# Performance work log

Measured on AMD Instinct MI355X. Metric: run time of the kernel, lower is better.

The kernel has to match this reference:

```python
import jax, jax.numpy as jnp
import numpy as np

WS = 8      # window_size
NH = 4      # num_heads (fixed in module)

def setup_inputs() -> dict:
    key = jax.random.key(0)
    k1, k2, k3 = jax.random.split(key, 3)
    B, C, H, W = 8, 512, 128, 128
    x = jax.random.normal(k1, (B, C, H, W), dtype=jnp.float32)
    # nn.MultiheadAttention parameters (xavier-ish scale)
    w_in = jax.random.normal(k2, (3 * C, C), dtype=jnp.float32) * (1.0 / np.sqrt(C))
    b_in = jnp.zeros((3 * C,), dtype=jnp.float32)
    w_out = jax.random.normal(k3, (C, C), dtype=jnp.float32) * (1.0 / np.sqrt(C))
    b_out = jnp.zeros((C,), dtype=jnp.float32)
    return {"x": x, "w_in": w_in, "b_in": b_in, "w_out": w_out, "b_out": b_out}

def reference(x, w_in, b_in, w_out, b_out):
    B, C, H, W = x.shape
    Hw, Ww = H // WS, W // WS
    hd = C // NH
    # --- window partition: (B,C,H,W) -> (N, L, C), N = B*Hw*Ww, L = WS*WS ---
    xw = x.reshape(B, C, Hw, WS, Ww, WS)
    xw = xw.transpose(0, 2, 4, 1, 3, 5)            # (B,Hw,Ww,C,WS,WS)
    xw = xw.reshape(-1, C, WS * WS)                # (N, C, L)
    xw = xw.transpose(0, 2, 1)                     # (N, L, C)
    N, L, _ = xw.shape
    # --- fused QKV projection (torch MultiheadAttention in_proj) ---
    qkv = jnp.einsum('nlc,ec->nle', xw, w_in) + b_in   # (N, L, 3C)
    q, k, v = jnp.split(qkv, 3, axis=-1)
    q = q.reshape(N, L, NH, hd)
    k = k.reshape(N, L, NH, hd)
    v = v.reshape(N, L, NH, hd)
    scale = 1.0 / np.sqrt(hd)
    scores = jnp.einsum('nqhd,nkhd->nhqk', q, k) * scale   # (N,NH,L,L)
    attn = jax.nn.softmax(scores, axis=-1)
    ctx = jnp.einsum('nhqk,nkhd->nqhd', attn, v).reshape(N, L, C)
    out = jnp.einsum('nlc,oc->nlo', ctx, w_out) + b_out    # (N, L, C)
    # --- window merge: (N,L,C) -> (B,C,H,W) ---
    out = out.transpose(0, 2, 1)                           # (N, C, L)
    out = out.reshape(B, Hw, Ww, C, WS, WS)
    out = out.transpose(0, 3, 1, 4, 2, 5)                  # (B,C,Hw,WS,Ww,WS)
    return out.reshape(B, C, H, W)
```

## Files before the change

### kernel.cpp

```cpp
#include <hip/hip_runtime.h>


typedef __attribute__((ext_vector_type(8))) short s16x8;
typedef __attribute__((ext_vector_type(4))) float f32x4;

#define C_TOT 512
#define HWIMG 128
#define CH_STRIDE (HWIMG * HWIMG)
#define NWIN 2048
#define XW_ELEMS ((size_t)NWIN * 64 * 512)
#define XW_BYTES (XW_ELEMS * 2ull)
#define WIT_ELEMS 786432ull
#define WOT_ELEMS 262144ull
#define WBF_ELEMS 1048576ull
#define WBF_BYTES (WBF_ELEMS * 2ull)
#define CTX_BYTES_FULL (XW_ELEMS * 2ull)

__device__ __forceinline__ unsigned short f2bf(float f) {
  unsigned u = __float_as_uint(f);
  u += 0x7FFFu + ((u >> 16) & 1u);
  return (unsigned short)(u >> 16);
}

__device__ __forceinline__ void gload_lds16(const void* g, void* l) {
  __builtin_amdgcn_global_load_lds(
      (const __attribute__((address_space(1))) unsigned int*)g,
      (__attribute__((address_space(3))) unsigned int*)l, 16, 0, 0);
}

__global__ void conv_w_kernel(const float* __restrict__ w_in,
                              const float* __restrict__ w_out,
                              unsigned short* __restrict__ wbf) {
  int i = blockIdx.x * blockDim.x + threadIdx.x;
  const int NIN = 3 * C_TOT * C_TOT;
  float v = (i < NIN) ? w_in[i] : w_out[i - NIN];
  wbf[i] = f2bf(v);
}

__global__ void conv_wt_kernel(const float* __restrict__ w_in,
                               const float* __restrict__ w_out,
                               unsigned short* __restrict__ wit,
                               unsigned short* __restrict__ wot) {
  int i = blockIdx.x * blockDim.x + threadIdx.x;
  const int NIN = 3 * C_TOT * C_TOT;
  if (i < NIN) {
    const int e = i >> 9, c = i & 511;
    const int t = e >> 9, rem = e & 511;
    const int h = rem >> 7, d = rem & 127;
    const int m = t * 8 + (d >> 4), l = d & 15;
    const int c8 = c >> 3, ec = c & 7;
    wit[(((size_t)(h * 24 + m) * 64 + c8) << 7) + l * 8 + ec] = f2bf(w_in[i]);
  } else {
    const int j = i - NIN;
    const int od = j >> 9, c = j & 511;
    const int m = od >> 4, l = od & 15;
    const int c8 = c >> 3, ec = c & 7;
    wot[(((size_t)m * 64 + c8) << 7) + l * 8 + ec] = f2bf(w_out[j]);
  }
}

__global__ void __launch_bounds__(256)
pack_x_kernel(const float* __restrict__ x, unsigned short* __restrict__ xw) {
  const int blk = blockIdx.x;
  const int bb  = blk >> 8;
  const int hw  = (blk >> 4) & 15;
  const int og4 = blk & 15;
  const int t   = threadIdx.x;
  const int p0  = 4 * t;
  const int r   = p0 >> 7;
  const int col0 = p0 & 127;
  const int n   = bb * 256 + hw * 16 + (col0 >> 3);
  const int tok0 = r * 8 + (col0 & 7);
  const float* xs = x + (size_t)bb * C_TOT * CH_STRIDE
                  + (size_t)hw * 1024 + p0;
  unsigned short* pw = xw + (size_t)n * 32768;
#pragma unroll
  for (int jo = 0; jo < 4; ++jo) {
    const int o = og4 * 4 + jo;
    float4 f[8];
#pragma unroll
    for (int k = 0; k < 8; ++k)
      f[k] = *(const float4*)(xs + (size_t)(8 * o + k) * CH_STRIDE);
#pragma unroll
    for (int i = 0; i < 4; ++i) {
      s16x8 pk;
      pk[0] = (short)f2bf(f[0].x); pk[1] = (short)f2bf(f[1].x);
      pk[2] = (short)f2bf(f[2].x); pk[3] = (short)f2bf(f[3].x);
      pk[4] = (short)f2bf(f[4].x); pk[5] = (short)f2bf(f[5].x);
      pk[6] = (short)f2bf(f[6].x); pk[7] = (short)f2bf(f[7].x);
      if (i == 0) {
        pk[0]=(short)f2bf(f[0].x); pk[1]=(short)f2bf(f[1].x); pk[2]=(short)f2bf(f[2].x); pk[3]=(short)f2bf(f[3].x);
        pk[4]=(short)f2bf(f[4].x); pk[5]=(short)f2bf(f[5].x); pk[6]=(short)f2bf(f[6].x); pk[7]=(short)f2bf(f[7].x);
      } else if (i == 1) {
        pk[0]=(short)f2bf(f[0].y); pk[1]=(short)f2bf(f[1].y); pk[2]=(short)f2bf(f[2].y); pk[3]=(short)f2bf(f[3].y);
        pk[4]=(short)f2bf(f[4].y); pk[5]=(short)f2bf(f[5].y); pk[6]=(short)f2bf(f[6].y); pk[7]=(short)f2bf(f[7].y);
      } else if (i == 2) {
        pk[0]=(short)f2bf(f[0].z); pk[1]=(short)f2bf(f[1].z); pk[2]=(short)f2bf(f[2].z); pk[3]=(short)f2bf(f[3].z);
        pk[4]=(short)f2bf(f[4].z); pk[5]=(short)f2bf(f[5].z); pk[6]=(short)f2bf(f[6].z); pk[7]=(short)f2bf(f[7].z);
      } else {
        pk[0]=(short)f2bf(f[0].w); pk[1]=(short)f2bf(f[1].w); pk[2]=(short)f2bf(f[2].w); pk[3]=(short)f2bf(f[3].w);
        pk[4]=(short)f2bf(f[4].w); pk[5]=(short)f2bf(f[5].w); pk[6]=(short)f2bf(f[6].w); pk[7]=(short)f2bf(f[7].w);
      }
      *(s16x8*)(pw + ((size_t)o * 64 + tok0 + i) * 8) = pk;
    }
  }
}

#define BQO 0
#define BKO 16384
#define BVO 32768
#define BXS 49152
#define BPO 49152
#define BLDS 81920

__global__ void __launch_bounds__(512, 4)
qkv_attn_kernel(const unsigned short* __restrict__ xw,
                const float* __restrict__ bin,
                const unsigned short* __restrict__ wit,
                unsigned short* __restrict__ ctx,
                int n0) {
  __shared__ __align__(16) unsigned char sm[BLDS];

  const int tid  = threadIdx.x;
  const int wv   = tid >> 6;
  const int lane = tid & 63;
  const int l15  = lane & 15;
  const int qd   = lane >> 4;
  const int swA  = (l15 & 7) << 4;

  const int blk = blockIdx.x;
  const int g   = blk & 7;
  const int q   = blk >> 3;
  const int h   = q & 3;
  const int nrel = (q >> 2) * 8 + g;
  const unsigned short* xww = xw + (size_t)(n0 + nrel) * 32768;

  const float SCALE = 0.08838834764831845f;
  const float L2E   = 1.4426950408889634f;

  f32x4 acc[3][4];
#pragma unroll
  for (int a = 0; a < 3; ++a)
#pragma unroll
    for (int b2 = 0; b2 < 4; ++b2) acc[a][b2] = (f32x4){0.f, 0.f, 0.f, 0.f};

  const unsigned short* arow[3];
  int typ[3], d128s[3];
#pragma unroll
  for (int mi = 0; mi < 3; ++mi) {
    const int d0 = 48 * wv + 16 * mi;
    const int t = d0 >> 7;
    const int d128 = d0 & 127;
    typ[mi] = t; d128s[mi] = d128;
    const int m = t * 8 + (d128 >> 4);
    arow[mi] = wit + ((size_t)(h * 24 + m) << 13) + l15 * 8;
  }

#pragma unroll
  for (int p = 0; p < 2; ++p)
    gload_lds16(xww + p * 4096 + tid * 8, &sm[BXS + p * 8192 + (wv << 10)]);
  __syncthreads();

  for (int s = 0; s < 4; ++s) {
    if (s < 3) {
#pragma unroll
      for (int p = 0; p < 2; ++p)
        gload_lds16(xww + (size_t)(s + 1) * 8192 + p * 4096 + tid * 8,
                    &sm[BXS + ((s + 1) & 1) * 16384 + p * 8192 + (wv << 10)]);
    }
    const int cur = BXS + (s & 1) * 16384;
#pragma unroll
    for (int j = 0; j < 4; ++j) {
      const int c8g = 16 * s + 4 * j + qd;
      const int lb = cur + ((4 * j + qd) << 10);
      s16x8 bx[4];
#pragma unroll
      for (int ni = 0; ni < 4; ++ni)
        bx[ni] = *(const s16x8*)(&sm[lb + (16 * ni + l15) * 16]);
#pragma unroll
      for (int mi = 0; mi < 3; ++mi) {
        const s16x8 af = *(const s16x8*)(arow[mi] + ((size_t)c8g << 7));
#pragma unroll
        for (int ni = 0; ni < 4; ++ni)
          acc[mi][ni] = __builtin_amdgcn_mfma_f32_16x16x32_bf16(af, bx[ni], acc[mi][ni], 0, 0, 0);
      }
    }
    __syncthreads();
  }

#pragma unroll
  for (int mi = 0; mi < 3; ++mi) {
    const int t = typ[mi], d128 = d128s[mi];
    const int e0 = t * 512 + h * 128 + d128 + 4 * qd;
    const float bi0 = bin[e0], bi1 = bin[e0 + 1], bi2 = bin[e0 + 2], bi3 = bin[e0 + 3];
#pragma unroll
    for (int ni = 0; ni < 4; ++ni) {
      const int tok = 16 * ni + l15;
      const unsigned short h0 = f2bf(acc[mi][ni][0] + bi0);
      const unsigned short h1 = f2bf(acc[mi][ni][1] + bi1);
      const unsigned short h2 = f2bf(acc[mi][ni][2] + bi2);
      const unsigned short h3 = f2bf(acc[mi][ni][3] + bi3);
      if (t < 2) {
        const unsigned lo = (unsigned)h0 | ((unsigned)h1 << 16);
        const unsigned hi = (unsigned)h2 | ((unsigned)h3 << 16);
        const unsigned long long pk = (unsigned long long)lo | ((unsigned long long)hi << 32);
        const int base = (t == 0) ? BQO : BKO;
        *(unsigned long long*)(&sm[base + tok * 256 + ((2 * (d128 + 4 * qd)) ^ swA)]) = pk;
      } else {
        const int vd = d128 + 4 * qd;
        *(unsigned short*)(&sm[BVO + (vd    ) * 128 + ((2 * tok) ^ (((vd    ) & 7) << 4))]) = h0;
        *(unsigned short*)(&sm[BVO + (vd + 1) * 128 + ((2 * tok) ^ (((vd + 1) & 7) << 4))]) = h1;
        *(unsigned short*)(&sm[BVO + (vd + 2) * 128 + ((2 * tok) ^ (((vd + 2) & 7) << 4))]) = h2;
        *(unsigned short*)(&sm[BVO + (vd + 3) * 128 + ((2 * tok) ^ (((vd + 3) & 7) << 4))]) = h3;
      }
    }
  }
  __syncthreads();

  if (wv < 4) {
    f32x4 s[4];
#pragma unroll
    for (int a = 0; a < 4; ++a) s[a] = (f32x4){0.f, 0.f, 0.f, 0.f};
    const int tqa = 16 * wv + l15;
#pragma unroll
    for (int ks = 0; ks < 4; ++ks) {
      const int c0 = 32 * ks + 8 * qd;
      const s16x8 aq = *(const s16x8*)(&sm[BQO + tqa * 256 + ((2 * c0) ^ swA)]);
#pragma unroll
      for (int ni = 0; ni < 4; ++ni) {
        const int tk = 16 * ni + l15;
        const s16x8 bk = *(const s16x8*)(&sm[BKO + tk * 256 + ((2 * c0) ^ swA)]);
        s[ni] = __builtin_amdgcn_mfma_f32_16x16x32_bf16(aq, bk, s[ni], 0, 0, 0);
      }
    }
    float sv[4][4];
#pragma unroll
    for (int ni = 0; ni < 4; ++ni)
#pragma unroll
      for (int i = 0; i < 4; ++i) sv[ni][i] = s[ni][i] * SCALE;
    float m[4];
#pragma unroll
    for (int i = 0; i < 4; ++i)
      m[i] = fmaxf(fmaxf(sv[0][i], sv[1][i]), fmaxf(sv[2][i], sv[3][i]));
#pragma unroll
    for (int d = 1; d < 16; d <<= 1)
#pragma unroll
      for (int i = 0; i < 4; ++i) m[i] = fmaxf(m[i], __shfl_xor(m[i], d));
    float p[4][4], sum[4] = {0.f, 0.f, 0.f, 0.f};
#pragma unroll
    for (int ni = 0; ni < 4; ++ni)
#pragma unroll
      for (int i = 0; i < 4; ++i) {
        p[ni][i] = exp2f((sv[ni][i] - m[i]) * L2E);
        sum[i] += p[ni][i];
      }
#pragma unroll
    for (int d = 1; d < 16; d <<= 1)
#pragma unroll
      for (int i = 0; i < 4; ++i) sum[i] += __shfl_xor(sum[i], d);
    float rinv[4];
#pragma unroll
    for (int i = 0; i < 4; ++i) rinv[i] = 1.0f / sum[i];
#pragma unroll
    for (int ni = 0; ni < 4; ++ni)
#pragma unroll
      for (int i = 0; i < 4; ++i) {
        const int tqr = 16 * wv + 4 * qd + i;
        const int tk = 16 * ni + l15;
        *(unsigned short*)(&sm[BPO + tqr * 128 + ((2 * tk) ^ ((tqr & 7) << 4))]) =
            f2bf(p[ni][i] * rinv[i]);
      }
  }
  __syncthreads();

  {
    const int mq = wv >> 1;
    const int nb = (wv & 1) * 4;
    f32x4 cacc[4];
#pragma unroll
    for (int a = 0; a < 4; ++a) cacc[a] = (f32x4){0.f, 0.f, 0.f, 0.f};
    const int tqa = 16 * mq + l15;
#pragma unroll
    for (int ks = 0; ks < 2; ++ks) {
      const int c0 = 32 * ks + 8 * qd;
      const s16x8 ap = *(const s16x8*)(&sm[BPO + tqa * 128 + ((2 * c0) ^ swA)]);
#pragma unroll
      for (int j = 0; j < 4; ++j) {
        const int vda = 16 * (nb + j) + l15;
        const s16x8 bv = *(const s16x8*)(&sm[BVO + vda * 128 + ((2 * c0) ^ swA)]);
        cacc[j] = __builtin_amdgcn_mfma_f32_16x16x32_bf16(ap, bv, cacc[j], 0, 0, 0);
      }
    }
    unsigned short* ctxn = ctx + (size_t)nrel * 32768;
#pragma unroll
    for (int j = 0; j < 4; ++j) {
      const int vd = 16 * (nb + j) + l15;
      const int c  = h * 128 + vd;
      const int c8 = c >> 3, e = c & 7;
#pragma unroll
      for (int i = 0; i < 4; ++i) {
        const int tq = 16 * mq + 4 * qd + i;
        ctxn[((size_t)c8 * 64 + tq) * 8 + e] = f2bf(cacc[j][i]);
      }
    }
  }
}

#define OXS 0
#define OLDS 32768

__global__ void __launch_bounds__(512, 4)
outproj_kernel(const unsigned short* __restrict__ ctx,
               const unsigned short* __restrict__ wot,
               const float* __restrict__ bout,
               float* __restrict__ out, int n0) {
  __shared__ __align__(16) unsigned char sm[OLDS];

  const int tid  = threadIdx.x;
  const int wv   = tid >> 6;
  const int lane = tid & 63;
  const int l15  = lane & 15;
  const int qd   = lane >> 4;

  const int nrel = blockIdx.x;
  const int n  = n0 + nrel;
  const int bb = n >> 8, hw = (n >> 4) & 15, ww = n & 15;
  const size_t wbase = (size_t)bb * C_TOT * CH_STRIDE
                     + (size_t)(hw * 8) * HWIMG + (size_t)(ww * 8);
  const unsigned short* ctxn = ctx + (size_t)nrel * 32768;

  f32x4 oacc[4][4];
#pragma unroll
  for (int a = 0; a < 4; ++a)
#pragma unroll
    for (int b2 = 0; b2 < 4; ++b2) oacc[a][b2] = (f32x4){0.f, 0.f, 0.f, 0.f};

  const unsigned short* orow[4];
#pragma unroll
  for (int mo = 0; mo < 4; ++mo)
    orow[mo] = wot + ((size_t)(4 * wv + mo) << 13) + l15 * 8;

#pragma unroll
  for (int p = 0; p < 2; ++p)
    gload_lds16(ctxn + p * 4096 + tid * 8, &sm[OXS + p * 8192 + (wv << 10)]);
  __syncthreads();

  for (int s = 0; s < 4; ++s) {
    if (s < 3) {
#pragma unroll
      for (int p = 0; p < 2; ++p)
        gload_lds16(ctxn + (size_t)(s + 1) * 8192 + p * 4096 + tid * 8,
                    &sm[OXS + ((s + 1) & 1) * 16384 + p * 8192 + (wv << 10)]);
    }
    const int cur = OXS + (s & 1) * 16384;
#pragma unroll
    for (int j = 0; j < 4; ++j) {
      const int c8g = 16 * s + 4 * j + qd;
      const int lb = cur + ((4 * j + qd) << 10);
      s16x8 bc[4];
#pragma unroll
      for (int ni = 0; ni < 4; ++ni)
        bc[ni] = *(const s16x8*)(&sm[lb + (16 * ni + l15) * 16]);
#pragma unroll
      for (int mo = 0; mo < 4; ++mo) {
        const s16x8 af = *(const s16x8*)(orow[mo] + ((size_t)c8g << 7));
#pragma unroll
        for (int ni = 0; ni < 4; ++ni)
          oacc[mo][ni] = __builtin_amdgcn_mfma_f32_16x16x32_bf16(af, bc[ni], oacc[mo][ni], 0, 0, 0);
      }
    }
    __syncthreads();
  }

#pragma unroll
  for (int mo = 0; mo < 4; ++mo) {
    const int od0 = 64 * wv + 16 * mo + 4 * qd;
    float bo[4];
#pragma unroll
    for (int i = 0; i < 4; ++i) bo[i] = bout[od0 + i];
#pragma unroll
    for (int ni = 0; ni < 4; ++ni) {
      const int tok = 16 * ni + l15;
      const int r = tok >> 3, cc = tok & 7;
#pragma unroll
      for (int i = 0; i < 4; ++i) {
        out[wbase + (size_t)(od0 + i) * CH_STRIDE + (size_t)r * HWIMG + cc] =
            oacc[mo][ni][i] + bo[i];
      }
    }
  }
}

#define QO    0
#define KO    16384
#define VO    32768
#define PO    49152
#define CTXO  57344
#define LDSB  73728

__global__ void __launch_bounds__(256)
pack_x_fb(const float* __restrict__ x, unsigned short* __restrict__ xw) {
  const int n  = blockIdx.x;
  const int bb = n >> 8, hw = (n >> 4) & 15, ww = n & 15;
  const size_t wbase = (size_t)bb * C_TOT * CH_STRIDE
                     + (size_t)(hw * 8) * HWIMG + (size_t)(ww * 8);
  const int tok = threadIdx.x & 63;
  const int q4  = threadIdx.x >> 6;
  const int r = tok >> 3, cc = tok & 7;
  const float* px = x + wbase + (size_t)r * HWIMG + cc;
  unsigned short* pw = xw + (size_t)n * 32768;
#pragma unroll 4
  for (int j = 0; j < 16; ++j) {
    const int o = q4 * 16 + j;
    float v[8];
#pragma unroll
    for (int k = 0; k < 8; ++k) v[k] = px[(size_t)(8 * o + k) * CH_STRIDE];
    s16x8 pk;
#pragma unroll
    for (int k = 0; k < 8; ++k) pk[k] = (short)f2bf(v[k]);
    *(s16x8*)(pw + ((size_t)o * 64 + tok) * 8) = pk;
  }
}

__global__ void __launch_bounds__(512, 2)
local_attn_kernel(const unsigned short* __restrict__ xw,
                  const float* __restrict__ bin,
                  const float* __restrict__ bout,
                  const unsigned short* __restrict__ wi,
                  const unsigned short* __restrict__ wo,
                  float* __restrict__ out) {
  __shared__ __align__(16) unsigned char sm[LDSB];
  const int tid  = threadIdx.x;
  const int wv   = tid >> 6;
  const int lane = tid & 63;
  const int l15  = lane & 15;
  const int qd   = lane >> 4;
  const int swA  = (l15 & 7) << 4;
  const int n  = blockIdx.x;
  const int bb = n >> 8;
  const int hw = (n >> 4) & 15;
  const int ww = n & 15;
  const size_t wbase = (size_t)bb * C_TOT * CH_STRIDE
                     + (size_t)(hw * 8) * HWIMG + (size_t)(ww * 8);
  const unsigned short* xww = xw + (size_t)n * 32768;
  f32x4 oacc[4][4];
#pragma unroll
  for (int a = 0; a < 4; ++a)
#pragma unroll
    for (int b2 = 0; b2 < 4; ++b2) oacc[a][b2] = (f32x4){0.f, 0.f, 0.f, 0.f};
  const float SCALE = 0.08838834764831845f;
  const float L2E   = 1.4426950408889634f;
  for (int h = 0; h < 4; ++h) {
    f32x4 acc[3][4];
#pragma unroll
    for (int a = 0; a < 3; ++a)
#pragma unroll
      for (int b2 = 0; b2 < 4; ++b2) acc[a][b2] = (f32x4){0.f, 0.f, 0.f, 0.f};
    const unsigned short* arow[3];
    int typ[3], d128s[3];
#pragma unroll
    for (int mi = 0; mi < 3; ++mi) {
      const int d0 = 48 * wv + 16 * mi;
      const int t = d0 >> 7;
      const int d128 = d0 & 127;
      typ[mi] = t; d128s[mi] = d128;
      arow[mi] = wi + (size_t)(t * 512 + h * 128 + d128 + l15) * 512;
    }
#pragma unroll 4
    for (int ks = 0; ks < 16; ++ks) {
      const int c0 = 32 * ks + 8 * qd;
      const int c8 = c0 >> 3;
      s16x8 bx[4];
#pragma unroll
      for (int ni = 0; ni < 4; ++ni)
        bx[ni] = *(const s16x8*)(xww + ((size_t)c8 * 64 + 16 * ni + l15) * 8);
#pragma unroll
      for (int mi = 0; mi < 3; ++mi) {
        const s16x8 af = *(const s16x8*)(arow[mi] + c0);
#pragma unroll
        for (int ni = 0; ni < 4; ++ni)
          acc[mi][ni] = __builtin_amdgcn_mfma_f32_16x16x32_bf16(af, bx[ni], acc[mi][ni], 0, 0, 0);
      }
    }
#pragma unroll
    for (int mi = 0; mi < 3; ++mi) {
      const int t = typ[mi], d128 = d128s[mi];
      const int e0 = t * 512 + h * 128 + d128 + 4 * qd;
      const float bi0 = bin[e0], bi1 = bin[e0 + 1], bi2 = bin[e0 + 2], bi3 = bin[e0 + 3];
#pragma unroll
      for (int ni = 0; ni < 4; ++ni) {
        const int tok = 16 * ni + l15;
        const unsigned short h0 = f2bf(acc[mi][ni][0] + bi0);
        const unsigned short h1 = f2bf(acc[mi][ni][1] + bi1);
        const unsigned short h2 = f2bf(acc[mi][ni][2] + bi2);
        const unsigned short h3 = f2bf(acc[mi][ni][3] + bi3);
        if (t < 2) {
          const unsigned lo = (unsigned)h0 | ((unsigned)h1 << 16);
          const unsigned hi = (unsigned)h2 | ((unsigned)h3 << 16);
          const unsigned long long pk = (unsigned long long)lo | ((unsigned long long)hi << 32);
          const int base = (t == 0) ? QO : KO;
          *(unsigned long long*)(&sm[base + tok * 256 + ((2 * (d128 + 4 * qd)) ^ swA)]) = pk;
        } else {
          const int vd = d128 + 4 * qd;
          *(unsigned short*)(&sm[VO + (vd    ) * 128 + ((2 * tok) ^ (((vd    ) & 7) << 4))]) = h0;
          *(unsigned short*)(&sm[VO + (vd + 1) * 128 + ((2 * tok) ^ (((vd + 1) & 7) << 4))]) = h1;
          *(unsigned short*)(&sm[VO + (vd + 2) * 128 + ((2 * tok) ^ (((vd + 2) & 7) << 4))]) = h2;
          *(unsigned short*)(&sm[VO + (vd + 3) * 128 + ((2 * tok) ^ (((vd + 3) & 7) << 4))]) = h3;
        }
      }
    }
    __syncthreads();
    if (wv < 4) {
      f32x4 s[4];
#pragma unroll
      for (int a = 0; a < 4; ++a) s[a] = (f32x4){0.f, 0.f, 0.f, 0.f};
      const int tqa = 16 * wv + l15;
#pragma unroll
      for (int ks = 0; ks < 4; ++ks) {
        const int c0 = 32 * ks + 8 * qd;
        const s16x8 aq = *(const s16x8*)(&sm[QO + tqa * 256 + ((2 * c0) ^ swA)]);
#pragma unroll
        for (int ni = 0; ni < 4; ++ni) {
          const int tk = 16 * ni + l15;
          const s16x8 bk = *(const s16x8*)(&sm[KO + tk * 256 + ((2 * c0) ^ swA)]);
          s[ni] = __builtin_amdgcn_mfma_f32_16x16x32_bf16(aq, bk, s[ni], 0, 0, 0);
        }
      }
      float sv[4][4];
#pragma unroll
      for (int ni = 0; ni < 4; ++ni)
#pragma unroll
        for (int i = 0; i < 4; ++i) sv[ni][i] = s[ni][i] * SCALE;
      float m[4];
#pragma unroll
      for (int i = 0; i < 4; ++i)
        m[i] = fmaxf(fmaxf(sv[0][i], sv[1][i]), fmaxf(sv[2][i], sv[3][i]));
#pragma unroll
      for (int d = 1; d < 16; d <<= 1)
#pragma unroll
        for (int i = 0; i < 4; ++i) m[i] = fmaxf(m[i], __shfl_xor(m[i], d));
      float p[4][4], sum[4] = {0.f, 0.f, 0.f, 0.f};
#pragma unroll
      for (int ni = 0; ni < 4; ++ni)
#pragma unroll
        for (int i = 0; i < 4; ++i) {
          p[ni][i] = exp2f((sv[ni][i] - m[i]) * L2E);
          sum[i] += p[ni][i];
        }
#pragma unroll
      for (int d = 1; d < 16; d <<= 1)
#pragma unroll
        for (int i = 0; i < 4; ++i) sum[i] += __shfl_xor(sum[i], d);
      float rinv[4];
#pragma unroll
      for (int i = 0; i < 4; ++i) rinv[i] = 1.0f / sum[i];
#pragma unroll
      for (int ni = 0; ni < 4; ++ni)
#pragma unroll
        for (int i = 0; i < 4; ++i) {
          const int tqr = 16 * wv + 4 * qd + i;
          const int tk = 16 * ni + l15;
          *(unsigned short*)(&sm[PO + tqr * 128 + ((2 * tk) ^ ((tqr & 7) << 4))]) =
              f2bf(p[ni][i] * rinv[i]);
        }
    }
    __syncthreads();
    {
      const int mq = wv >> 1;
      const int nb = (wv & 1) * 4;
      f32x4 cacc[4];
#pragma unroll
      for (int a = 0; a < 4; ++a) cacc[a] = (f32x4){0.f, 0.f, 0.f, 0.f};
      const int tqa = 16 * mq + l15;
#pragma unroll
      for (int ks = 0; ks < 2; ++ks) {
        const int c0 = 32 * ks + 8 * qd;
        const s16x8 ap = *(const s16x8*)(&sm[PO + tqa * 128 + ((2 * c0) ^ swA)]);
#pragma unroll
        for (int j = 0; j < 4; ++j) {
          const int vda = 16 * (nb + j) + l15;
          const s16x8 bv = *(const s16x8*)(&sm[VO + vda * 128 + ((2 * c0) ^ swA)]);
          cacc[j] = __builtin_amdgcn_mfma_f32_16x16x32_bf16(ap, bv, cacc[j], 0, 0, 0);
        }
      }
#pragma unroll
      for (int j = 0; j < 4; ++j)
#pragma unroll
        for (int i = 0; i < 4; ++i) {
          const int tq = 16 * mq + 4 * qd + i;
          const int vd = 16 * (nb + j) + l15;
          *(unsigned short*)(&sm[CTXO + tq * 256 + ((2 * vd) ^ ((tq & 7) << 4))]) =
              f2bf(cacc[j][i]);
        }
    }
    __syncthreads();
    {
#pragma unroll
      for (int ks = 0; ks < 4; ++ks) {
        const int c0 = 32 * ks + 8 * qd;
        s16x8 a2[4];
#pragma unroll
        for (int mo = 0; mo < 4; ++mo) {
          const int od = 64 * wv + 16 * mo + l15;
          a2[mo] = *(const s16x8*)(&wo[(size_t)od * 512 + 128 * h + c0]);
        }
        s16x8 bc[4];
#pragma unroll
        for (int ni = 0; ni < 4; ++ni) {
          const int tok = 16 * ni + l15;
          bc[ni] = *(const s16x8*)(&sm[CTXO + tok * 256 + ((2 * c0) ^ swA)]);
        }
#pragma unroll
        for (int mo = 0; mo < 4; ++mo)
#pragma unroll
          for (int ni = 0; ni < 4; ++ni)
            oacc[mo][ni] = __builtin_amdgcn_mfma_f32_16x16x32_bf16(a2[mo], bc[ni], oacc[mo][ni], 0, 0, 0);
      }
    }
  }
#pragma unroll
  for (int mo = 0; mo < 4; ++mo) {
    const int od0 = 64 * wv + 16 * mo + 4 * qd;
    float bo[4];
#pragma unroll
    for (int i = 0; i < 4; ++i) bo[i] = bout[od0 + i];
#pragma unroll
    for (int ni = 0; ni < 4; ++ni) {
      const int tok = 16 * ni + l15;
      const int r = tok >> 3, cc = tok & 7;
#pragma unroll
      for (int i = 0; i < 4; ++i) {
        out[wbase + (size_t)(od0 + i) * CH_STRIDE + (size_t)r * HWIMG + cc] =
            oacc[mo][ni][i] + bo[i];
      }
    }
  }
}

extern "C" void kernel_launch(void* const* d_in, const int* in_sizes, int n_in,
                              void* d_out, int out_size, void* d_ws, size_t ws_size,
                              hipStream_t stream) {
  const float* x     = (const float*)d_in[0];
  const float* w_in  = (const float*)d_in[1];
  const float* b_in  = (const float*)d_in[2];
  const float* w_out = (const float*)d_in[3];
  const float* b_out = (const float*)d_in[4];
  float* out = (float*)d_out;

  const size_t TIL_BYTES = (WIT_ELEMS + WOT_ELEMS) * 2ull;
  int nc = 0;
  for (int c = 1; c <= 8; c <<= 1) {
    if (ws_size >= XW_BYTES + TIL_BYTES + CTX_BYTES_FULL / (size_t)c) { nc = c; break; }
  }

  if (nc) {
    unsigned short* xwp = (unsigned short*)d_ws;
    unsigned short* wit = xwp + XW_ELEMS;
    unsigned short* wot = wit + WIT_ELEMS;
    unsigned short* ctx = wot + WOT_ELEMS;
    conv_wt_kernel<<<4096, 256, 0, stream>>>(w_in, w_out, wit, wot);
    pack_x_kernel<<<2048, 256, 0, stream>>>(x, xwp);
    const int nwc = NWIN / nc;
    for (int k = 0; k < nc; ++k) {
      qkv_attn_kernel<<<nwc * 4, 512, 0, stream>>>(xwp, b_in, wit, ctx, k * nwc);
      outproj_kernel<<<nwc, 512, 0, stream>>>(ctx, wot, b_out, out, k * nwc);
    }
  } else {
    unsigned short* xwp = (unsigned short*)d_ws;
    unsigned short* wbf = xwp + XW_ELEMS;
    conv_w_kernel<<<4096, 256, 0, stream>>>(w_in, w_out, wbf);
    pack_x_fb<<<NWIN, 256, 0, stream>>>(x, xwp);
    local_attn_kernel<<<NWIN, 512, 0, stream>>>(xwp, b_in, b_out,
                                                wbf, wbf + 786432, out);
  }
}
```

Before: 591.2 us.

## Spread QK^T and softmax across all eight waves via LDS score staging

```diff
diff --git a/kernel.cpp b/kernel.cpp
--- a/kernel.cpp
+++ b/kernel.cpp
@@ -13,7 +13,6 @@
 #define WIT_ELEMS 786432ull
 #define WOT_ELEMS 262144ull
 #define WBF_ELEMS 1048576ull
-#define WBF_BYTES (WBF_ELEMS * 2ull)
 #define CTX_BYTES_FULL (XW_ELEMS * 2ull)
 
 __device__ __forceinline__ unsigned short f2bf(float f) {
@@ -84,10 +83,6 @@
 #pragma unroll
     for (int i = 0; i < 4; ++i) {
       s16x8 pk;
-      pk[0] = (short)f2bf(f[0].x); pk[1] = (short)f2bf(f[1].x);
-      pk[2] = (short)f2bf(f[2].x); pk[3] = (short)f2bf(f[3].x);
-      pk[4] = (short)f2bf(f[4].x); pk[5] = (short)f2bf(f[5].x);
-      pk[6] = (short)f2bf(f[6].x); pk[7] = (short)f2bf(f[7].x);
       if (i == 0) {
         pk[0]=(short)f2bf(f[0].x); pk[1]=(short)f2bf(f[1].x); pk[2]=(short)f2bf(f[2].x); pk[3]=(short)f2bf(f[3].x);
         pk[4]=(short)f2bf(f[4].x); pk[5]=(short)f2bf(f[5].x); pk[6]=(short)f2bf(f[6].x); pk[7]=(short)f2bf(f[7].x);
@@ -111,6 +106,7 @@
 #define BVO 32768
 #define BXS 49152
 #define BPO 49152
+#define BSO 57344
 #define BLDS 81920
 
 __global__ void __launch_bounds__(512, 4)
@@ -217,59 +213,58 @@
   }
   __syncthreads();
 
-  if (wv < 4) {
-    f32x4 s[4];
-#pragma unroll
-    for (int a = 0; a < 4; ++a) s[a] = (f32x4){0.f, 0.f, 0.f, 0.f};
-    const int tqa = 16 * wv + l15;
+  {
+    const int mq  = wv >> 1;
+    const int nk0 = (wv & 1) * 2;
+    f32x4 s[2];
+#pragma unroll
+    for (int a = 0; a < 2; ++a) s[a] = (f32x4){0.f, 0.f, 0.f, 0.f};
+    const int tqa = 16 * mq + l15;
 #pragma unroll
     for (int ks = 0; ks < 4; ++ks) {
       const int c0 = 32 * ks + 8 * qd;
       const s16x8 aq = *(const s16x8*)(&sm[BQO + tqa * 256 + ((2 * c0) ^ swA)]);
 #pragma unroll
-      for (int ni = 0; ni < 4; ++ni) {
-        const int tk = 16 * ni + l15;
-        const s16x8 bk = *(const s16x8*)(&sm[BKO + tk * 256 + ((2 * c0) ^ swA)]);
-        s[ni] = __builtin_amdgcn_mfma_f32_16x16x32_bf16(aq, bk, s[ni], 0, 0, 0);
-      }
-    }
-    float sv[4][4];
-#pragma unroll
-    for (int ni = 0; ni < 4; ++ni)
-#pragma unroll
-      for (int i = 0; i < 4; ++i) sv[ni][i] = s[ni][i] * SCALE;
-    float m[4];
-#pragma unroll
-    for (int i = 0; i < 4; ++i)
-      m[i] = fmaxf(fmaxf(sv[0][i], sv[1][i]), fmaxf(sv[2][i], sv[3][i]));
-#pragma unroll
-    for (int d = 1; d < 16; d <<= 1)
-#pragma unroll
-      for (int i = 0; i < 4; ++i) m[i] = fmaxf(m[i], __shfl_xor(m[i], d));
-    float p[4][4], sum[4] = {0.f, 0.f, 0.f, 0.f};
-#pragma unroll
-    for (int ni = 0; ni < 4; ++ni)
+      for (int j = 0; j < 2; ++j) {
+        const int tka = 16 * (nk0 + j) + l15;
+        const s16x8 bk = *(const s16x8*)(&sm[BKO + tka * 256 + ((2 * c0) ^ swA)]);
+        s[j] = __builtin_amdgcn_mfma_f32_16x16x32_bf16(aq, bk, s[j], 0, 0, 0);
+      }
+    }
+#pragma unroll
+    for (int j = 0; j < 2; ++j)
 #pragma unroll
       for (int i = 0; i < 4; ++i) {
-        p[ni][i] = exp2f((sv[ni][i] - m[i]) * L2E);
-        sum[i] += p[ni][i];
-      }
-#pragma unroll
-    for (int d = 1; d < 16; d <<= 1)
-#pragma unroll
-      for (int i = 0; i < 4; ++i) sum[i] += __shfl_xor(sum[i], d);
-    float rinv[4];
-#pragma unroll
-    for (int i = 0; i < 4; ++i) rinv[i] = 1.0f / sum[i];
-#pragma unroll
-    for (int ni = 0; ni < 4; ++ni)
-#pragma unroll
-      for (int i = 0; i < 4; ++i) {
-        const int tqr = 16 * wv + 4 * qd + i;
-        const int tk = 16 * ni + l15;
-        *(unsigned short*)(&sm[BPO + tqr * 128 + ((2 * tk) ^ ((tqr & 7) << 4))]) =
-            f2bf(p[ni][i] * rinv[i]);
-      }
+        const int tq = 16 * mq + 4 * qd + i;
+        const int tk = 16 * (nk0 + j) + l15;
+        *(float*)(&sm[BSO + tq * 256 + ((4 * tk) ^ ((tq & 7) << 4))]) = s[j][i] * SCALE;
+      }
+  }
+  __syncthreads();
+
+#pragma unroll
+  for (int half = 0; half < 2; ++half) {
+    const int r = 8 * wv + 2 * qd + half;
+    float v[4];
+#pragma unroll
+    for (int j = 0; j < 4; ++j)
+      v[j] = *(const float*)(&sm[BSO + r * 256 + ((4 * (16 * j + l15)) ^ ((r & 7) << 4))]);
+    float m = fmaxf(fmaxf(v[0], v[1]), fmaxf(v[2], v[3]));
+#pragma unroll
+    for (int d = 1; d < 16; d <<= 1) m = fmaxf(m, __shfl_xor(m, d));
+    float p[4], sum = 0.f;
+#pragma unroll
+    for (int j = 0; j < 4; ++j) {
+      p[j] = exp2f((v[j] - m) * L2E);
+      sum += p[j];
+    }
+#pragma unroll
+    for (int d = 1; d < 16; d <<= 1) sum += __shfl_xor(sum, d);
+    const float rinv = 1.0f / sum;
+#pragma unroll
+    for (int j = 0; j < 4; ++j)
+      *(unsigned short*)(&sm[BPO + r * 128 + ((2 * (16 * j + l15)) ^ ((r & 7) << 4))]) =
+          f2bf(p[j] * rinv);
   }
   __syncthreads();
 
```

Result: no change. 585.5 us (-1.0%).
